# Kernel optimization log

Hardware: AMD Instinct MI355X
Metric: run time of the kernel (lower is better)

The kernel has to match this reference:

```python
import jax, jax.numpy as jnp
import numpy as np

H = 256       # hidden_size
LAT = 32      # latent_size
AV = 40       # atom vocab size
NB = 4        # bond types
B = 256       # batch (num molecules)
LSRC = 400    # src graph length per molecule
NT = 38400    # topo predictions
NA = 38400    # atom predictions
NBD = 76800   # bond predictions


def _lin(key, fin, fout):
    k1, k2 = jax.random.split(key)
    s = 1.0 / np.sqrt(fin)
    w = jax.random.uniform(k1, (fout, fin), jnp.float32, -s, s)
    b = jax.random.uniform(k2, (fout,), jnp.float32, -s, s)
    return w, b


def setup_inputs() -> dict:
    key = jax.random.key(0)
    ks = jax.random.split(key, 24)
    d = {}
    d['src_graph_vecs'] = jax.random.normal(ks[0], (B, LSRC, LAT), jnp.float32)
    d['topo_vecs'] = jax.random.normal(ks[1], (NT, 2 * H), jnp.float32)
    d['atom_vecs'] = jax.random.normal(ks[2], (NA, 2 * H), jnp.float32)
    d['bond_vecs'] = jax.random.normal(ks[3], (NBD, 3 * H), jnp.float32)
    d['topo_idx'] = jax.random.randint(ks[4], (NT,), 0, B)
    d['atom_idx'] = jax.random.randint(ks[5], (NA,), 0, B)
    d['bond_idx'] = jax.random.randint(ks[6], (NBD,), 0, B)
    d['topo_labels'] = jax.random.randint(ks[7], (NT,), 0, 2)
    d['atom_labels'] = jax.random.randint(ks[8], (NA,), 0, AV)
    d['bond_labels'] = jax.random.randint(ks[9], (NBD,), 0, NB)
    d['A_topo_w'], d['A_topo_b'] = _lin(ks[10], 2 * H, LAT)
    d['A_atom_w'], d['A_atom_b'] = _lin(ks[11], 2 * H, LAT)
    d['A_bond_w'], d['A_bond_b'] = _lin(ks[12], 3 * H, LAT)
    d['topoNN_w1'], d['topoNN_b1'] = _lin(ks[13], 2 * H + LAT, H)
    d['topoNN_w2'], d['topoNN_b2'] = _lin(ks[14], H, 1)
    d['atomNN_w1'], d['atomNN_b1'] = _lin(ks[15], 2 * H + LAT, H)
    d['atomNN_w2'], d['atomNN_b2'] = _lin(ks[16], H, AV)
    d['bondNN_w1'], d['bondNN_b1'] = _lin(ks[17], 3 * H + LAT, H)
    d['bondNN_w2'], d['bondNN_b2'] = _lin(ks[18], H, NB)
    return d


def _attention(src, idx, q_in, Aw, Ab):
    # src: [B, L, LAT]; irregular gather per prediction row
    src_g = src[idx]                                   # [N, L, LAT]
    q = q_in @ Aw.T + Ab                               # [N, LAT]
    att = jax.nn.softmax(jnp.einsum('nld,nd->nl', src_g, q), axis=1)
    return jnp.einsum('nl,nld->nd', att, src_g)        # [N, LAT]


def _mlp(x, w1, b1, w2, b2):
    return jax.nn.relu(x @ w1.T + b1) @ w2.T + b2


def _ce_sum(logits, labels):
    lp = jax.nn.log_softmax(logits, axis=-1)
    return -jnp.sum(jnp.take_along_axis(lp, labels[:, None], axis=-1))


def reference(src_graph_vecs, topo_vecs, atom_vecs, bond_vecs,
              topo_idx, atom_idx, bond_idx,
              topo_labels, atom_labels, bond_labels,
              A_topo_w, A_topo_b, A_atom_w, A_atom_b, A_bond_w, A_bond_b,
              topoNN_w1, topoNN_b1, topoNN_w2, topoNN_b2,
              atomNN_w1, atomNN_b1, atomNN_w2, atomNN_b2,
              bondNN_w1, bondNN_b1, bondNN_w2, bondNN_b2):
    bsz = src_graph_vecs.shape[0]
    # topo head
    t_cxt = _attention(src_graph_vecs, topo_idx, topo_vecs, A_topo_w, A_topo_b)
    t_scores = _mlp(jnp.concatenate([topo_vecs, t_cxt], -1),
                    topoNN_w1, topoNN_b1, topoNN_w2, topoNN_b2)[:, 0]
    yt = topo_labels.astype(jnp.float32)
    topo_loss = jnp.sum(jax.nn.softplus(t_scores) - yt * t_scores)  # BCEWithLogits sum
    topo_acc = jnp.mean(((t_scores > 0).astype(jnp.int32) == topo_labels).astype(jnp.float32))
    # atom head
    a_cxt = _attention(src_graph_vecs, atom_idx, atom_vecs, A_atom_w, A_atom_b)
    a_scores = _mlp(jnp.concatenate([atom_vecs, a_cxt], -1),
                    atomNN_w1, atomNN_b1, atomNN_w2, atomNN_b2)
    atom_loss = _ce_sum(a_scores, atom_labels)
    atom_acc = jnp.mean((jnp.argmax(a_scores, -1) == atom_labels).astype(jnp.float32))
    # bond head
    b_cxt = _attention(src_graph_vecs, bond_idx, bond_vecs, A_bond_w, A_bond_b)
    b_scores = _mlp(jnp.concatenate([bond_vecs, b_cxt], -1),
                    bondNN_w1, bondNN_b1, bondNN_w2, bondNN_b2)
    bond_loss = _ce_sum(b_scores, bond_labels)
    bond_acc = jnp.mean((jnp.argmax(b_scores, -1) == bond_labels).astype(jnp.float32))
    loss = (topo_loss + atom_loss + bond_loss) / bsz
    return (loss, atom_acc, topo_acc, bond_acc)
```

## Files before the change

### kernel.cpp

```cpp
#include <hip/hip_runtime.h>
#include <math.h>

#define LATD 32
#define AV 40
#define NBOND 4
#define BATCH 256
#define LSRC 400
#define NT 38400
#define NA 38400
#define NBD 76800

typedef unsigned short ushort_t;
typedef short short8 __attribute__((ext_vector_type(8)));
typedef float f32x4 __attribute__((ext_vector_type(4)));
typedef unsigned short ushort4v __attribute__((ext_vector_type(4)));
typedef unsigned short ushort8v __attribute__((ext_vector_type(8)));

__device__ __forceinline__ ushort_t f2bf(float f) {
    union { float f; unsigned u; } v; v.f = f;
    unsigned r = v.u + 0x7fffu + ((v.u >> 16) & 1u);
    return (ushort_t)(r >> 16);
}
__device__ __forceinline__ float bf2f(ushort_t u) {
    union { unsigned u; float f; } v; v.u = ((unsigned)u) << 16;
    return v.f;
}

__global__ void init_kernel(float* acc, int* cnt) {
    int t = threadIdx.x;
    if (t < 8) acc[t] = 0.0f;
    cnt[t] = 0; cnt[t + 256] = 0; cnt[t + 512] = 0;
}

__global__ __launch_bounds__(256) void hist_kernel(const int* __restrict__ idx, int N,
                                                   int* __restrict__ cnt) {
    __shared__ int lc[256];
    int t = threadIdx.x;
    lc[t] = 0;
    __syncthreads();
    for (int i = blockIdx.x * 256 + t; i < N; i += gridDim.x * 256)
        atomicAdd(&lc[idx[i]], 1);
    __syncthreads();
    if (lc[t]) atomicAdd(&cnt[t], lc[t]);
}

__global__ __launch_bounds__(256) void scan_kernel(const int* __restrict__ cnt,
                                                   int* __restrict__ cur,
                                                   int* __restrict__ bstart) {
    __shared__ int s[256];
    int t = threadIdx.x;
    for (int h = 0; h < 3; ++h) {
        int v = cnt[h * 256 + t];
        s[t] = v;
        __syncthreads();
        for (int d = 1; d < 256; d <<= 1) {
            int u = (t >= d) ? s[t - d] : 0;
            __syncthreads();
            s[t] += u;
            __syncthreads();
        }
        cur[h * 256 + t] = s[t] - v;
        bstart[h * 256 + t] = s[t] - v;
        __syncthreads();
    }
}

__global__ __launch_bounds__(256) void scatter_kernel(const int* __restrict__ idx, int N,
                                                      int* __restrict__ cur,
                                                      int* __restrict__ bucket) {
    for (int i = blockIdx.x * 256 + threadIdx.x; i < N; i += gridDim.x * 256) {
        int b = idx[i];
        int p = atomicAdd(&cur[b], 1);
        bucket[p] = i;
    }
}

template<int DIN>
__global__ __launch_bounds__(256) void qproj_kernel(
    const float* __restrict__ X,
    const float* __restrict__ Aw,
    const float* __restrict__ Ab,
    ushort_t* __restrict__ Qbf)
{
    __shared__ ushort_t As[64 * 72];
    __shared__ ushort_t Bs[32 * 72];
    const int tid = threadIdx.x;
    const int wave = tid >> 6, lane = tid & 63;
    const int l15 = lane & 15, quad = lane >> 4;
    const int row0 = blockIdx.x * 64;

    const int ar = tid >> 2;
    const int ak = (tid & 3) * 8;
    const int br = tid >> 3;
    const int bk = (tid & 7) * 8;

    f32x4 acc0 = {0.f,0.f,0.f,0.f}, acc1 = {0.f,0.f,0.f,0.f};

    for (int k0 = 0; k0 < DIN; k0 += 64) {
        {
            const float* xb = X + (size_t)(row0 + ar) * DIN + k0 + ak;
            float4 v0 = *(const float4*)xb,        v1 = *(const float4*)(xb + 4);
            float4 v2 = *(const float4*)(xb + 32), v3 = *(const float4*)(xb + 36);
            ushort8v p;
            p[0]=f2bf(v0.x); p[1]=f2bf(v0.y); p[2]=f2bf(v0.z); p[3]=f2bf(v0.w);
            p[4]=f2bf(v1.x); p[5]=f2bf(v1.y); p[6]=f2bf(v1.z); p[7]=f2bf(v1.w);
            *(ushort8v*)&As[ar * 72 + ak] = p;
            p[0]=f2bf(v2.x); p[1]=f2bf(v2.y); p[2]=f2bf(v2.z); p[3]=f2bf(v2.w);
            p[4]=f2bf(v3.x); p[5]=f2bf(v3.y); p[6]=f2bf(v3.z); p[7]=f2bf(v3.w);
            *(ushort8v*)&As[ar * 72 + ak + 32] = p;
        }
        {
            const float* wb = Aw + (size_t)br * DIN + k0 + bk;
            float4 w0 = *(const float4*)wb, w1 = *(const float4*)(wb + 4);
            ushort8v p;
            p[0]=f2bf(w0.x); p[1]=f2bf(w0.y); p[2]=f2bf(w0.z); p[3]=f2bf(w0.w);
            p[4]=f2bf(w1.x); p[5]=f2bf(w1.y); p[6]=f2bf(w1.z); p[7]=f2bf(w1.w);
            *(ushort8v*)&Bs[br * 72 + bk] = p;
        }
        __syncthreads();
        short8 a0 = *(const short8*)&As[(wave*16 + l15) * 72 + quad*8];
        short8 a1 = *(const short8*)&As[(wave*16 + l15) * 72 + 32 + quad*8];
        short8 b0 = *(const short8*)&Bs[l15 * 72 + quad*8];
        short8 b1 = *(const short8*)&Bs[l15 * 72 + 32 + quad*8];
        short8 b2 = *(const short8*)&Bs[(16 + l15) * 72 + quad*8];
        short8 b3 = *(const short8*)&Bs[(16 + l15) * 72 + 32 + quad*8];
        acc0 = __builtin_amdgcn_mfma_f32_16x16x32_bf16(a0, b0, acc0, 0, 0, 0);
        acc0 = __builtin_amdgcn_mfma_f32_16x16x32_bf16(a1, b1, acc0, 0, 0, 0);
        acc1 = __builtin_amdgcn_mfma_f32_16x16x32_bf16(a0, b2, acc1, 0, 0, 0);
        acc1 = __builtin_amdgcn_mfma_f32_16x16x32_bf16(a1, b3, acc1, 0, 0, 0);
        __syncthreads();
    }
    const float ab0 = Ab[l15];
    const float ab1 = Ab[16 + l15];
#pragma unroll
    for (int r = 0; r < 4; ++r) {
        int row = row0 + wave*16 + quad*4 + r;
        Qbf[(size_t)row * 32 + l15]      = f2bf(acc0[r] + ab0);
        Qbf[(size_t)row * 32 + 16 + l15] = f2bf(acc1[r] + ab1);
    }
}

template<int TPB, int NBLK>
__global__ __launch_bounds__(256) void attn2_kernel(
    const float* __restrict__ src,
    const ushort_t* __restrict__ Qbf,
    const int* __restrict__ bucket,
    const int* __restrict__ bstart,
    const int* __restrict__ cnt,
    ushort_t* __restrict__ cxtb)
{
    const int m  = blockIdx.x / NBLK;
    const int t0 = (blockIdx.x % NBLK) * TPB;
    const int cm = cnt[m];
    if (t0 * 32 >= cm) return;

    __shared__ __align__(16) char smem[54272];
    ushort_t* sSrcT  = (ushort_t*)(smem);
    ushort_t* sP     = (ushort_t*)(smem + 26752);
    float*    sStats = (float*)(smem + 53632);
    int*      sRows  = (int*)(smem + 54144);

    const int tid = threadIdx.x;
    const int wave = tid >> 6, lane = tid & 63;
    const int l15 = lane & 15, quad = lane >> 4;
    const int mt = wave & 1;
    const int nt = wave >> 1;
    const bool full = (nt == 0);

    {
        const float4* s4 = (const float4*)(src + (size_t)m * (LSRC * LATD));
        for (int i = tid; i < 3200; i += 256) {
            float4 v = s4[i];
            int l = i >> 3, d4 = (i & 7) * 4;
            sSrcT[(d4 + 0) * 418 + l] = f2bf(v.x);
            sSrcT[(d4 + 1) * 418 + l] = f2bf(v.y);
            sSrcT[(d4 + 2) * 418 + l] = f2bf(v.z);
            sSrcT[(d4 + 3) * 418 + l] = f2bf(v.w);
        }
        for (int i = tid; i < 512; i += 256) {
            int d = i >> 4, l = 400 + (i & 15);
            sSrcT[d * 418 + l] = 0;
        }
        for (int i = tid; i < 512; i += 256) {
            int row = i >> 4, col = 400 + (i & 15);
            sP[row * 420 + col] = 0;
        }
    }
    __syncthreads();

    const int Tm = (cm + 31) >> 5;
    const int rem = Tm - t0;
    const int ntiles = rem < TPB ? rem : TPB;

    for (int tt = 0; tt < ntiles; ++tt) {
        const int t = t0 + tt;
        if (tid < 32) {
            int p = t * 32 + tid;
            sRows[tid] = (p < cm) ? bucket[bstart[m] + p] : -1;
        }
        __syncthreads();

        const int grow = sRows[mt * 16 + l15];
        short8 aq = {0,0,0,0,0,0,0,0};
        if (grow >= 0)
            aq = *(const short8*)(Qbf + (size_t)grow * 32 + quad * 8);

        f32x4 sc[13];
#pragma unroll
        for (int j = 0; j < 13; ++j) {
            int c = nt + 2 * j;
            int bbase = quad * 8 * 418 + c * 16 + l15;
            short8 bv;
#pragma unroll
            for (int e = 0; e < 8; ++e) bv[e] = (short)sSrcT[bbase + e * 418];
            f32x4 z = {0.f, 0.f, 0.f, 0.f};
            sc[j] = __builtin_amdgcn_mfma_f32_16x16x32_bf16(aq, bv, z, 0, 0, 0);
        }

        float Mr[4], Sr[4];
#pragma unroll
        for (int r = 0; r < 4; ++r) {
            float mx = sc[0][r];
#pragma unroll
            for (int j = 1; j < 12; ++j) mx = fmaxf(mx, sc[j][r]);
            if (full) mx = fmaxf(mx, sc[12][r]);
            float s = 0.f;
#pragma unroll
            for (int j = 0; j < 12; ++j) s += __expf(sc[j][r] - mx);
            if (full) s += __expf(sc[12][r] - mx);
            Mr[r] = mx; Sr[r] = s;
        }
#pragma unroll
        for (int msk = 1; msk < 16; msk <<= 1) {
#pragma unroll
            for (int r = 0; r < 4; ++r) {
                float mo = __shfl_xor(Mr[r], msk, 64);
                float so = __shfl_xor(Sr[r], msk, 64);
                float mn = fmaxf(Mr[r], mo);
                Sr[r] = Sr[r] * __expf(Mr[r] - mn) + so * __expf(mo - mn);
                Mr[r] = mn;
            }
        }
        if (l15 == 0) {
#pragma unroll
            for (int r = 0; r < 4; ++r) {
                sStats[(wave * 16 + quad * 4 + r) * 2 + 0] = Mr[r];
                sStats[(wave * 16 + quad * 4 + r) * 2 + 1] = Sr[r];
            }
        }
        __syncthreads();
        {
            const int pw = wave ^ 2;
#pragma unroll
            for (int r = 0; r < 4; ++r) {
                float mo = sStats[(pw * 16 + quad * 4 + r) * 2 + 0];
                float so = sStats[(pw * 16 + quad * 4 + r) * 2 + 1];
                float mn = fmaxf(Mr[r], mo);
                float L = Sr[r] * __expf(Mr[r] - mn) + so * __expf(mo - mn);
                Mr[r] = mn; Sr[r] = 1.0f / L;
            }
        }
#pragma unroll
        for (int j = 0; j < 12; ++j) {
            int col = (nt + 2 * j) * 16 + l15;
#pragma unroll
            for (int r = 0; r < 4; ++r) {
                int row = mt * 16 + quad * 4 + r;
                sP[row * 420 + col] = f2bf(__expf(sc[j][r] - Mr[r]) * Sr[r]);
            }
        }
        if (full) {
            int col = 24 * 16 + l15;
#pragma unroll
            for (int r = 0; r < 4; ++r) {
                int row = mt * 16 + quad * 4 + r;
                sP[row * 420 + col] = f2bf(__expf(sc[12][r] - Mr[r]) * Sr[r]);
            }
        }
        __syncthreads();

        f32x4 oac = {0.f, 0.f, 0.f, 0.f};
#pragma unroll
        for (int k0 = 0; k0 < 416; k0 += 32) {
            short8 ap = *(const short8*)&sP[(mt * 16 + l15) * 420 + k0 + quad * 8];
            short8 bp = *(const short8*)&sSrcT[(nt * 16 + l15) * 418 + k0 + quad * 8];
            oac = __builtin_amdgcn_mfma_f32_16x16x32_bf16(ap, bp, oac, 0, 0, 0);
        }
        {
            int col = nt * 16 + l15;
#pragma unroll
            for (int r = 0; r < 4; ++r) {
                int rowl = mt * 16 + quad * 4 + r;
                int g = sRows[rowl];
                if (g >= 0) cxtb[(size_t)g * 32 + col] = f2bf(oac[r]);
            }
        }
        __syncthreads();
    }
}

template<int DIN, int DO>
__global__ __launch_bounds__(256) void mlp_mfma_kernel(
    const float* __restrict__ X,
    const ushort_t* __restrict__ cxtb,
    const float* __restrict__ W1,
    const float* __restrict__ B1,
    const float* __restrict__ W2,
    const float* __restrict__ B2,
    const int* __restrict__ labels,
    float* __restrict__ accum,
    int M)
{
    constexpr int DC = DIN + 32;
    constexpr int KITERS = DC / 32;

    __shared__ ushort_t sAB[10240];
    __shared__ ushort_t HS[64 * 256];
    __shared__ float lg[64 * DO];

    ushort_t* As = sAB;
    ushort_t* Bs = sAB + 2048;

    const int tid = threadIdx.x;
    const int row0 = blockIdx.x * 64;
    const int wave = tid >> 6;
    const int lane = tid & 63;
    const int l15 = lane & 15;
    const int l4 = lane >> 4;

    f32x4 acc[4][4];
#pragma unroll
    for (int mi = 0; mi < 4; ++mi)
#pragma unroll
        for (int ni = 0; ni < 4; ++ni)
            acc[mi][ni] = (f32x4){0.f, 0.f, 0.f, 0.f};

    for (int it = 0; it < KITERS; ++it) {
        const int k0 = it * 32;
#pragma unroll
        for (int half = 0; half < 2; ++half) {
            int f = tid + half * 256;
            int row = f >> 3, k4 = (f & 7) * 4;
            ushort4v pk;
            if (k0 < DIN) {
                float4 v = *(const float4*)(X + (size_t)(row0 + row) * DIN + k0 + k4);
                pk[0] = f2bf(v.x); pk[1] = f2bf(v.y);
                pk[2] = f2bf(v.z); pk[3] = f2bf(v.w);
            } else {
                pk = *(const ushort4v*)(cxtb + (size_t)(row0 + row) * 32 + k4);
            }
            *(ushort4v*)&As[row * 32 + k4] = pk;
        }
#pragma unroll
        for (int i = 0; i < 8; ++i) {
            int f = tid + i * 256;
            int n = f >> 3, k4 = (f & 7) * 4;
            float4 v = *(const float4*)(W1 + (size_t)n * DC + k0 + k4);
            ushort4v pk;
            pk[0] = f2bf(v.x); pk[1] = f2bf(v.y);
            pk[2] = f2bf(v.z); pk[3] = f2bf(v.w);
            *(ushort4v*)&Bs[n * 32 + k4] = pk;
        }
        __syncthreads();

        short8 af[4], bfv[4];
#pragma unroll
        for (int mi = 0; mi < 4; ++mi)
            af[mi] = *(const short8*)&As[(mi * 16 + l15) * 32 + l4 * 8];
#pragma unroll
        for (int ni = 0; ni < 4; ++ni)
            bfv[ni] = *(const short8*)&Bs[(wave * 64 + ni * 16 + l15) * 32 + l4 * 8];
#pragma unroll
        for (int mi = 0; mi < 4; ++mi)
#pragma unroll
            for (int ni = 0; ni < 4; ++ni)
                acc[mi][ni] = __builtin_amdgcn_mfma_f32_16x16x32_bf16(
                    af[mi], bfv[ni], acc[mi][ni], 0, 0, 0);
        __syncthreads();
    }

    float b1v[4];
#pragma unroll
    for (int ni = 0; ni < 4; ++ni) b1v[ni] = B1[wave * 64 + ni * 16 + l15];
#pragma unroll
    for (int mi = 0; mi < 4; ++mi) {
#pragma unroll
        for (int ni = 0; ni < 4; ++ni) {
            int col = wave * 64 + ni * 16 + l15;
#pragma unroll
            for (int r = 0; r < 4; ++r) {
                int rowl = mi * 16 + l4 * 4 + r;
                float h = fmaxf(acc[mi][ni][r] + b1v[ni], 0.0f);
                HS[rowl * 256 + col] = f2bf(h);
            }
        }
    }
#pragma unroll 4
    for (int j = 0; j < DO; ++j)
        sAB[j * 256 + tid] = f2bf(W2[(size_t)j * 256 + tid]);
    __syncthreads();

    for (int p = tid; p < 64 * DO; p += 256) {
        int r = p / DO, o = p - (p / DO) * DO;
        float s = 0.0f;
#pragma unroll 4
        for (int kk = 0; kk < 32; ++kk) {
            ushort8v hv = *(const ushort8v*)&HS[r * 256 + kk * 8];
            ushort8v wv = *(const ushort8v*)&sAB[o * 256 + kk * 8];
#pragma unroll
            for (int e = 0; e < 8; ++e) s += bf2f(hv[e]) * bf2f(wv[e]);
        }
        lg[p] = s + B2[o];
    }
    __syncthreads();

    float loss_l = 0.0f, cnt_l = 0.0f;
    if (tid < 64) {
        int lab = labels[row0 + tid];
        if (DO == 1) {
            float s = lg[tid];
            loss_l = fmaxf(s, 0.0f) + log1pf(__expf(-fabsf(s))) - (float)lab * s;
            int pred = (s > 0.0f) ? 1 : 0;
            cnt_l = (pred == lab) ? 1.0f : 0.0f;
        } else {
            const float* lr = &lg[tid * DO];
            float mx = lr[0];
            int am = 0;
#pragma unroll
            for (int o = 1; o < DO; ++o) {
                float v = lr[o];
                if (v > mx) { mx = v; am = o; }
            }
            float se = 0.0f;
#pragma unroll
            for (int o = 0; o < DO; ++o) se += __expf(lr[o] - mx);
            loss_l = mx + logf(se) - lr[lab];
            cnt_l = (am == lab) ? 1.0f : 0.0f;
        }
#pragma unroll
        for (int off = 32; off > 0; off >>= 1) {
            loss_l += __shfl_down(loss_l, off, 64);
            cnt_l  += __shfl_down(cnt_l, off, 64);
        }
        if (tid == 0) {
            atomicAdd(accum, loss_l);
            atomicAdd(accum + 1, cnt_l);
        }
    }
}

__global__ void finalize_kernel(const float* __restrict__ acc, float* __restrict__ out) {
    if (threadIdx.x == 0) {
        out[0] = (acc[0] + acc[2] + acc[4]) / (float)BATCH;
        out[1] = acc[3] / (float)NA;
        out[2] = acc[1] / (float)NT;
        out[3] = acc[5] / (float)NBD;
    }
}

extern "C" void kernel_launch(void* const* d_in, const int* in_sizes, int n_in,
                              void* d_out, int out_size, void* d_ws, size_t ws_size,
                              hipStream_t stream) {
    const float* src      = (const float*)d_in[0];
    const float* topoX    = (const float*)d_in[1];
    const float* atomX    = (const float*)d_in[2];
    const float* bondX    = (const float*)d_in[3];
    const int*   topo_idx = (const int*)d_in[4];
    const int*   atom_idx = (const int*)d_in[5];
    const int*   bond_idx = (const int*)d_in[6];
    const int*   topo_lab = (const int*)d_in[7];
    const int*   atom_lab = (const int*)d_in[8];
    const int*   bond_lab = (const int*)d_in[9];
    const float* Atw = (const float*)d_in[10]; const float* Atb = (const float*)d_in[11];
    const float* Aaw = (const float*)d_in[12]; const float* Aab = (const float*)d_in[13];
    const float* Abw = (const float*)d_in[14]; const float* Abb = (const float*)d_in[15];
    const float* tW1 = (const float*)d_in[16]; const float* tB1 = (const float*)d_in[17];
    const float* tW2 = (const float*)d_in[18]; const float* tB2 = (const float*)d_in[19];
    const float* aW1 = (const float*)d_in[20]; const float* aB1 = (const float*)d_in[21];
    const float* aW2 = (const float*)d_in[22]; const float* aB2 = (const float*)d_in[23];
    const float* bW1 = (const float*)d_in[24]; const float* bB1 = (const float*)d_in[25];
    const float* bW2 = (const float*)d_in[26]; const float* bB2 = (const float*)d_in[27];
    float* out = (float*)d_out;

    char* ws = (char*)d_ws;
    float* acc    = (float*)ws;
    int*   cnt    = (int*)(ws + 256);
    int*   cur    = (int*)(ws + 3328);
    int*   bstart = (int*)(ws + 6400);
    int*   bkt_t  = (int*)(ws + 9472);
    int*   bkt_a  = bkt_t + NT;
    int*   bkt_b  = bkt_a + NA;
    ushort_t* cxtb = (ushort_t*)(ws + 623872);
    ushort_t* Qbf  = (ushort_t*)(ws + 5539072);

    hipLaunchKernelGGL(init_kernel, dim3(1), dim3(256), 0, stream, acc, cnt);

    hipLaunchKernelGGL(hist_kernel, dim3(128), dim3(256), 0, stream, topo_idx, NT, cnt + 0);
    hipLaunchKernelGGL(hist_kernel, dim3(128), dim3(256), 0, stream, atom_idx, NA, cnt + 256);
    hipLaunchKernelGGL(hist_kernel, dim3(128), dim3(256), 0, stream, bond_idx, NBD, cnt + 512);
    hipLaunchKernelGGL(scan_kernel, dim3(1), dim3(256), 0, stream, cnt, cur, bstart);
    hipLaunchKernelGGL(scatter_kernel, dim3(256), dim3(256), 0, stream, topo_idx, NT, cur + 0, bkt_t);
    hipLaunchKernelGGL(scatter_kernel, dim3(256), dim3(256), 0, stream, atom_idx, NA, cur + 256, bkt_a);
    hipLaunchKernelGGL(scatter_kernel, dim3(256), dim3(256), 0, stream, bond_idx, NBD, cur + 512, bkt_b);

    hipLaunchKernelGGL((qproj_kernel<512>), dim3(NT / 64), dim3(256), 0, stream,
                       topoX, Atw, Atb, Qbf);
    hipLaunchKernelGGL((attn2_kernel<4, 3>), dim3(256 * 3), dim3(256), 0, stream,
                       src, Qbf, bkt_t, bstart + 0, cnt + 0, cxtb);
    hipLaunchKernelGGL((mlp_mfma_kernel<512, 1>), dim3(NT / 64), dim3(256), 0, stream,
                       topoX, cxtb, tW1, tB1, tW2, tB2, topo_lab, acc + 0, NT);

    hipLaunchKernelGGL((qproj_kernel<512>), dim3(NA / 64), dim3(256), 0, stream,
                       atomX, Aaw, Aab, Qbf);
    hipLaunchKernelGGL((attn2_kernel<4, 3>), dim3(256 * 3), dim3(256), 0, stream,
                       src, Qbf, bkt_a, bstart + 256, cnt + 256, cxtb);
    hipLaunchKernelGGL((mlp_mfma_kernel<512, 40>), dim3(NA / 64), dim3(256), 0, stream,
                       atomX, cxtb, aW1, aB1, aW2, aB2, atom_lab, acc + 2, NA);

    hipLaunchKernelGGL((qproj_kernel<768>), dim3(NBD / 64), dim3(256), 0, stream,
                       bondX, Abw, Abb, Qbf);
    hipLaunchKernelGGL((attn2_kernel<5, 4>), dim3(256 * 4), dim3(256), 0, stream,
                       src, Qbf, bkt_b, bstart + 512, cnt + 512, cxtb);
    hipLaunchKernelGGL((mlp_mfma_kernel<768, 4>), dim3(NBD / 64), dim3(256), 0, stream,
                       bondX, cxtb, bW1, bB1, bW2, bB2, bond_lab, acc + 4, NBD);

    hipLaunchKernelGGL(finalize_kernel, dim3(1), dim3(64), 0, stream, acc, out);
}
```

Before: 1.179 ms.

## Pre-convert MLP weights to bf16, pad LDS strides, use MFMA for second layer

Adds a small conversion kernel that turns the W1/W2 weights of each MLP head into bf16 once per call, so each MLP block loads bf16 weights directly instead of converting fp32 per tile. LDS row strides are padded (36, 264, 49) to reduce bank conflicts. The scalar second-layer dot products are replaced by MFMA 16x16x32 over padded output tiles. This adds six small launches and a workspace region, and reuses shared memory between phases.

```diff
diff --git a/kernel.cpp b/kernel.cpp
--- a/kernel.cpp
+++ b/kernel.cpp
@@ -30,6 +30,17 @@
     int t = threadIdx.x;
     if (t < 8) acc[t] = 0.0f;
     cnt[t] = 0; cnt[t + 256] = 0; cnt[t + 512] = 0;
+}
+
+__global__ __launch_bounds__(256) void convbf_kernel(const float* __restrict__ in,
+                                                     ushort_t* __restrict__ out, int n4) {
+    int i = blockIdx.x * 256 + threadIdx.x;
+    if (i < n4) {
+        float4 v = ((const float4*)in)[i];
+        ushort4v p;
+        p[0] = f2bf(v.x); p[1] = f2bf(v.y); p[2] = f2bf(v.z); p[3] = f2bf(v.w);
+        ((ushort4v*)out)[i] = p;
+    }
 }
 
 __global__ __launch_bounds__(256) void hist_kernel(const int* __restrict__ idx, int N,
@@ -303,9 +314,9 @@
 __global__ __launch_bounds__(256) void mlp_mfma_kernel(
     const float* __restrict__ X,
     const ushort_t* __restrict__ cxtb,
-    const float* __restrict__ W1,
+    const ushort_t* __restrict__ W1bf,
     const float* __restrict__ B1,
-    const float* __restrict__ W2,
+    const ushort_t* __restrict__ W2bf,
     const float* __restrict__ B2,
     const int* __restrict__ labels,
     float* __restrict__ accum,
@@ -313,13 +324,17 @@
 {
     constexpr int DC = DIN + 32;
     constexpr int KITERS = DC / 32;
-
-    __shared__ ushort_t sAB[10240];
-    __shared__ ushort_t HS[64 * 256];
-    __shared__ float lg[64 * DO];
-
-    ushort_t* As = sAB;
-    ushort_t* Bs = sAB + 2048;
+    constexpr int ASTR = 36;
+    constexpr int HSW = 264;
+    constexpr int LGW = 49;
+    constexpr int NT2 = (DO + 15) / 16;
+
+    __shared__ __align__(16) char smem[59136];
+    ushort_t* As  = (ushort_t*)smem;
+    ushort_t* Bs  = (ushort_t*)(smem + 4608);
+    ushort_t* HS  = (ushort_t*)smem;
+    ushort_t* W2s = (ushort_t*)(smem + 33792);
+    float*    lg  = (float*)(smem + 33792);
 
     const int tid = threadIdx.x;
     const int row0 = blockIdx.x * 64;
@@ -327,6 +342,13 @@
     const int lane = tid & 63;
     const int l15 = lane & 15;
     const int l4 = lane >> 4;
+
+    for (int f = tid; f < NT2 * 16 * 32; f += 256) {
+        int n = f >> 5, kc = (f & 31) * 8;
+        ushort8v v = (ushort8v){0,0,0,0,0,0,0,0};
+        if (n < DO) v = *(const ushort8v*)&W2bf[n * 256 + kc];
+        *(ushort8v*)&W2s[n * HSW + kc] = v;
+    }
 
     f32x4 acc[4][4];
 #pragma unroll
@@ -349,27 +371,24 @@
             } else {
                 pk = *(const ushort4v*)(cxtb + (size_t)(row0 + row) * 32 + k4);
             }
-            *(ushort4v*)&As[row * 32 + k4] = pk;
-        }
-#pragma unroll
-        for (int i = 0; i < 8; ++i) {
+            *(ushort4v*)&As[row * ASTR + k4] = pk;
+        }
+#pragma unroll
+        for (int i = 0; i < 4; ++i) {
             int f = tid + i * 256;
-            int n = f >> 3, k4 = (f & 7) * 4;
-            float4 v = *(const float4*)(W1 + (size_t)n * DC + k0 + k4);
-            ushort4v pk;
-            pk[0] = f2bf(v.x); pk[1] = f2bf(v.y);
-            pk[2] = f2bf(v.z); pk[3] = f2bf(v.w);
-            *(ushort4v*)&Bs[n * 32 + k4] = pk;
+            int n = f >> 2, kc = (f & 3) * 8;
+            *(ushort8v*)&Bs[n * ASTR + kc] =
+                *(const ushort8v*)&W1bf[(size_t)n * DC + k0 + kc];
         }
         __syncthreads();
 
         short8 af[4], bfv[4];
 #pragma unroll
         for (int mi = 0; mi < 4; ++mi)
-            af[mi] = *(const short8*)&As[(mi * 16 + l15) * 32 + l4 * 8];
+            af[mi] = *(const short8*)&As[(mi * 16 + l15) * ASTR + l4 * 8];
 #pragma unroll
         for (int ni = 0; ni < 4; ++ni)
-            bfv[ni] = *(const short8*)&Bs[(wave * 64 + ni * 16 + l15) * 32 + l4 * 8];
+            bfv[ni] = *(const short8*)&Bs[(wave * 64 + ni * 16 + l15) * ASTR + l4 * 8];
 #pragma unroll
         for (int mi = 0; mi < 4; ++mi)
 #pragma unroll
@@ -391,26 +410,35 @@
             for (int r = 0; r < 4; ++r) {
                 int rowl = mi * 16 + l4 * 4 + r;
                 float h = fmaxf(acc[mi][ni][r] + b1v[ni], 0.0f);
-                HS[rowl * 256 + col] = f2bf(h);
-            }
-        }
-    }
-#pragma unroll 4
-    for (int j = 0; j < DO; ++j)
-        sAB[j * 256 + tid] = f2bf(W2[(size_t)j * 256 + tid]);
+                HS[rowl * HSW + col] = f2bf(h);
+            }
+        }
+    }
     __syncthreads();
 
-    for (int p = tid; p < 64 * DO; p += 256) {
-        int r = p / DO, o = p - (p / DO) * DO;
-        float s = 0.0f;
-#pragma unroll 4
-        for (int kk = 0; kk < 32; ++kk) {
-            ushort8v hv = *(const ushort8v*)&HS[r * 256 + kk * 8];
-            ushort8v wv = *(const ushort8v*)&sAB[o * 256 + kk * 8];
-#pragma unroll
-            for (int e = 0; e < 8; ++e) s += bf2f(hv[e]) * bf2f(wv[e]);
-        }
-        lg[p] = s + B2[o];
+    f32x4 acc2[NT2];
+#pragma unroll
+    for (int nti = 0; nti < NT2; ++nti) acc2[nti] = (f32x4){0.f, 0.f, 0.f, 0.f};
+#pragma unroll
+    for (int kk = 0; kk < 256; kk += 32) {
+        short8 af2 = *(const short8*)&HS[(wave * 16 + l15) * HSW + kk + l4 * 8];
+#pragma unroll
+        for (int nti = 0; nti < NT2; ++nti) {
+            short8 bf2 = *(const short8*)&W2s[(nti * 16 + l15) * HSW + kk + l4 * 8];
+            acc2[nti] = __builtin_amdgcn_mfma_f32_16x16x32_bf16(af2, bf2, acc2[nti], 0, 0, 0);
+        }
+    }
+    __syncthreads();
+
+#pragma unroll
+    for (int nti = 0; nti < NT2; ++nti) {
+        int col = nti * 16 + l15;
+        if (col < DO) {
+            float b2 = B2[col];
+#pragma unroll
+            for (int r = 0; r < 4; ++r)
+                lg[(wave * 16 + l4 * 4 + r) * LGW + col] = acc2[nti][r] + b2;
+        }
     }
     __syncthreads();
 
@@ -418,12 +446,12 @@
     if (tid < 64) {
         int lab = labels[row0 + tid];
         if (DO == 1) {
-            float s = lg[tid];
+            float s = lg[tid * LGW];
             loss_l = fmaxf(s, 0.0f) + log1pf(__expf(-fabsf(s))) - (float)lab * s;
             int pred = (s > 0.0f) ? 1 : 0;
             cnt_l = (pred == lab) ? 1.0f : 0.0f;
         } else {
-            const float* lr = &lg[tid * DO];
+            const float* lr = &lg[tid * LGW];
             float mx = lr[0];
             int am = 0;
 #pragma unroll
@@ -492,8 +520,21 @@
     int*   bkt_b  = bkt_a + NA;
     ushort_t* cxtb = (ushort_t*)(ws + 623872);
     ushort_t* Qbf  = (ushort_t*)(ws + 5539072);
+    ushort_t* w1t  = (ushort_t*)(ws + 10454272);
+    ushort_t* w1a  = (ushort_t*)(ws + 10732800);
+    ushort_t* w1b  = (ushort_t*)(ws + 11011328);
+    ushort_t* w2t  = (ushort_t*)(ws + 11420928);
+    ushort_t* w2a  = (ushort_t*)(ws + 11421440);
+    ushort_t* w2b  = (ushort_t*)(ws + 11441920);
 
     hipLaunchKernelGGL(init_kernel, dim3(1), dim3(256), 0, stream, acc, cnt);
+
+    hipLaunchKernelGGL(convbf_kernel, dim3((256*544/4 + 255)/256), dim3(256), 0, stream, tW1, w1t, 256*544/4);
+    hipLaunchKernelGGL(convbf_kernel, dim3((256*544/4 + 255)/256), dim3(256), 0, stream, aW1, w1a, 256*544/4);
+    hipLaunchKernelGGL(convbf_kernel, dim3((256*800/4 + 255)/256), dim3(256), 0, stream, bW1, w1b, 256*800/4);
+    hipLaunchKernelGGL(convbf_kernel, dim3(1), dim3(256), 0, stream, tW2, w2t, 256/4);
+    hipLaunchKernelGGL(convbf_kernel, dim3((40*256/4 + 255)/256), dim3(256), 0, stream, aW2, w2a, 40*256/4);
+    hipLaunchKernelGGL(convbf_kernel, dim3(1), dim3(256), 0, stream, bW2, w2b, 4*256/4);
 
     hipLaunchKernelGGL(hist_kernel, dim3(128), dim3(256), 0, stream, topo_idx, NT, cnt + 0);
     hipLaunchKernelGGL(hist_kernel, dim3(128), dim3(256), 0, stream, atom_idx, NA, cnt + 256);
@@ -508,21 +549,21 @@
     hipLaunchKernelGGL((attn2_kernel<4, 3>), dim3(256 * 3), dim3(256), 0, stream,
                        src, Qbf, bkt_t, bstart + 0, cnt + 0, cxtb);
     hipLaunchKernelGGL((mlp_mfma_kernel<512, 1>), dim3(NT / 64), dim3(256), 0, stream,
-                       topoX, cxtb, tW1, tB1, tW2, tB2, topo_lab, acc + 0, NT);
+                       topoX, cxtb, w1t, tB1, w2t, tB2, topo_lab, acc + 0, NT);
 
     hipLaunchKernelGGL((qproj_kernel<512>), dim3(NA / 64), dim3(256), 0, stream,
                        atomX, Aaw, Aab, Qbf);
     hipLaunchKernelGGL((attn2_kernel<4, 3>), dim3(256 * 3), dim3(256), 0, stream,
                        src, Qbf, bkt_a, bstart + 256, cnt + 256, cxtb);
     hipLaunchKernelGGL((mlp_mfma_kernel<512, 40>), dim3(NA / 64), dim3(256), 0, stream,
-                       atomX, cxtb, aW1, aB1, aW2, aB2, atom_lab, acc + 2, NA);
+                       atomX, cxtb, w1a, aB1, w2a, aB2, atom_lab, acc + 2, NA);
 
     hipLaunchKernelGGL((qproj_kernel<768>), dim3(NBD / 64), dim3(256), 0, stream,
                        bondX, Abw, Abb, Qbf);
     hipLaunchKernelGGL((attn2_kernel<5, 4>), dim3(256 * 4), dim3(256), 0, stream,
                        src, Qbf, bkt_b, bstart + 512, cnt + 512, cxtb);
     hipLaunchKernelGGL((mlp_mfma_kernel<768, 4>), dim3(NBD / 64), dim3(256), 0, stream,
-                       bondX, cxtb, bW1, bB1, bW2, bB2, bond_lab, acc + 4, NBD);
+                       bondX, cxtb, w1b, bB1, w2b, bB2, bond_lab, acc + 4, NBD);
 
     hipLaunchKernelGGL(finalize_kernel, dim3(1), dim3(64), 0, stream, acc, out);
 }
```

Result: slower. 1.224 ms (+3.8%).
